# Performance work log

Measured on AMD Instinct MI355X. Metric: run time of the kernel, lower is better.

Reference implementation:

```python
import jax, jax.numpy as jnp
import numpy as np
from jax import lax

ALPHA = 2.0
T_TAGS = 8  # number of distinct connects tags
ANCHOR_POS_FACTOR = jnp.array([1.0, 1.0], dtype=jnp.float32)
POS_FACTOR = [2.0, 1.0]  # [4,4,4,2,1][-2:]
NEG_FACTOR = [2.0, 1.0]


def setup_inputs() -> dict:
    key = jax.random.key(0)
    ks = jax.random.split(key, 10)
    B, A, M = 2, 2, 64
    Da, Db = 128, 64
    logits_a = jax.random.normal(ks[0], (B, A, Da, Da, Da), dtype=jnp.float32)
    logits_b = jax.random.normal(ks[1], (B, A, Db, Db, Db), dtype=jnp.float32)
    # GT prob maps: background labeled -1 (negmask), sparse positives labeled 1
    prob_a = jnp.where(jax.random.uniform(ks[2], (B, A, Da, Da, Da)) < 0.995, -1.0, 1.0).astype(jnp.float32)
    prob_b = jnp.where(jax.random.uniform(ks[3], (B, A, Db, Db, Db)) < 0.995, -1.0, 1.0).astype(jnp.float32)
    connects_a = jax.random.randint(ks[4], (B, A, Da, Da, Da), 0, T_TAGS, dtype=jnp.int32)
    connects_b = jax.random.randint(ks[5], (B, A, Db, Db, Db), 0, T_TAGS, dtype=jnp.int32)
    def make_coord(k, D):
        ka, kz = jax.random.split(k)
        anc = jax.random.randint(ka, (B, M, 1), 0, A, dtype=jnp.int32)
        sp = jax.random.randint(kz, (B, M, 3), 0, D, dtype=jnp.int32)
        c = jnp.concatenate([anc, sp], axis=-1)
        # pad last quarter of rows with -1 (invalid), as in the original padded coord lists
        c = c.at[:, 3 * M // 4:, :].set(-1)
        return c
    coord_a = make_coord(ks[6], Da)
    coord_b = make_coord(ks[7], Db)
    fnames = jnp.arange(B, dtype=jnp.float32)
    return {"logits_a": logits_a, "logits_b": logits_b, "prob_a": prob_a, "prob_b": prob_b,
            "connects_a": connects_a, "connects_b": connects_b,
            "coord_a": coord_a, "coord_b": coord_b, "fnames": fnames}


def _level_loss(logits, prob_gt, connects, coord, pos_f, neg_f):
    # ---- negative branch: sigmoid/logsigmoid elementwise + NMS maxpool mask ----
    prob = jax.nn.sigmoid(logits)
    nll = -jax.nn.log_sigmoid(-logits)  # -log(1 - sigmoid(logit))
    negmask = (prob_gt == -1.0).astype(logits.dtype)
    # max_pool3d kernel 3, stride 1, pad 1 over (D,H,W); anchors are channels
    pooled = lax.reduce_window(prob, -jnp.inf, lax.max,
                               (1, 1, 3, 3, 3), (1, 1, 1, 1, 1), 'SAME')
    max_filter = lax.stop_gradient((pooled == prob).astype(logits.dtype))
    negmask = negmask * max_filter
    w_neg = lax.stop_gradient(prob) ** ALPHA * negmask
    loss_neg = jnp.sum(nll * w_neg) * neg_f
    count_neg = jnp.sum(w_neg)
    wsum_neg = jnp.sum(w_neg) * neg_f

    # ---- positive branch: batched gather at coords (pad rows = -1) ----
    B, M, _ = coord.shape
    valid = coord[:, :, 0] > -1                       # [B, M]
    c = jnp.where(valid[..., None], coord, 0)         # safe indices
    b_idx = jnp.arange(B)[:, None]
    lp = logits[b_idx, c[..., 0], c[..., 1], c[..., 2], c[..., 3]]  # [B, M]
    pp = jax.nn.sigmoid(lp)
    w1 = (1.0 - lax.stop_gradient(pp)) ** ALPHA
    w2 = ANCHOR_POS_FACTOR[c[..., 0]]
    vf = valid.astype(logits.dtype)
    loss_pos = -jnp.sum(jax.nn.log_sigmoid(lp) * w1 * w2 * vf) * pos_f
    count_pos = jnp.sum(w1 * vf)
    wsum_pos = jnp.sum(w1 * w2 * vf) * pos_f

    # ---- connects-tag segment-min grouping (torch.unique + per-tag min) ----
    tags = connects[b_idx, c[..., 0], c[..., 1], c[..., 2], c[..., 3]]  # [B, M]
    seg = (jnp.arange(B, dtype=jnp.int32)[:, None] * T_TAGS + tags).reshape(-1)
    data = jnp.where(valid, w1, jnp.inf).reshape(-1)
    seg_min = jax.ops.segment_min(data, seg, num_segments=B * T_TAGS).reshape(B, T_TAGS)
    seg_min = jnp.where(jnp.isfinite(seg_min), seg_min, -1.0)  # absent tags -> -1 sentinel
    return loss_pos, loss_neg, count_pos, count_neg, wsum_pos, wsum_neg, seg_min


def reference(logits_a, logits_b, prob_a, prob_b, connects_a, connects_b, coord_a, coord_b, fnames):
    ra = _level_loss(logits_a, prob_a, connects_a, coord_a, POS_FACTOR[0], NEG_FACTOR[0])
    rb = _level_loss(logits_b, prob_b, connects_b, coord_b, POS_FACTOR[1], NEG_FACTOR[1])
    cls_loss_pos = ra[0] + rb[0]
    cls_loss_neg = ra[1] + rb[1]
    count_pos = ra[2] + rb[2]
    count_neg = ra[3] + rb[3]
    wsum_pos = ra[4] + rb[4]
    wsum_neg = ra[5] + rb[5]
    # pred_prob summary: per (level, sample, tag) min positive weight; fnames broadcast alongside
    pred_prob_min = jnp.stack([ra[6], rb[6]], axis=0)  # [2, B, T_TAGS]
    return (cls_loss_pos, cls_loss_neg, count_pos, count_neg, wsum_pos, wsum_neg, pred_prob_min)
```

## Files before the change

kernel.cpp:

```cpp
#include <hip/hip_runtime.h>
#include <math.h>


#define NBLK_A 1024
#define NBLK_B 128
#define NBLK_TOTAL (NBLK_A + NBLK_B + 1)

__device__ __forceinline__ float fmax3(float a, float b, float c) {
    return fmaxf(a, fmaxf(b, c));
}

template <int D, int LOG2D, int XQ>
__device__ __forceinline__ void neg_march(
    const float* __restrict__ logits, const float* __restrict__ gt,
    int vol, int z, int y0, int xq, float& loss, float& wsum)
{
    const int x0 = xq << 2;
    const float* vb = logits + (vol << (3 * LOG2D));
    const int zm = z > 0 ? z - 1 : 0;
    const int zp = z < D - 1 ? z + 1 : z;
    const float* pzm = vb + (zm << (2 * LOG2D));
    const float* pz0 = vb + (z << (2 * LOG2D));
    const float* pzp = vb + (zp << (2 * LOG2D));
    const float* pg = gt + (vol << (3 * LOG2D)) + (z << (2 * LOG2D));

    float zw[3][4];
    float cc[2][4];
    float4 gg[2];

#pragma unroll
    for (int s = 0; s < 10; ++s) {
        int yy = y0 - 1 + s;
        yy = yy < 0 ? 0 : (yy > D - 1 ? D - 1 : yy);
        const int ro = (yy << LOG2D) + x0;
        float4 r0 = *(const float4*)(pzm + ro);
        float4 r1 = *(const float4*)(pz0 + ro);
        float4 r2 = *(const float4*)(pzp + ro);
        if (s >= 1 && s <= 8) gg[s & 1] = *(const float4*)(pg + ro);
        zw[s % 3][0] = fmax3(r0.x, r1.x, r2.x);
        zw[s % 3][1] = fmax3(r0.y, r1.y, r2.y);
        zw[s % 3][2] = fmax3(r0.z, r1.z, r2.z);
        zw[s % 3][3] = fmax3(r0.w, r1.w, r2.w);
        cc[s & 1][0] = r1.x; cc[s & 1][1] = r1.y;
        cc[s & 1][2] = r1.z; cc[s & 1][3] = r1.w;
        if (s >= 2) {
            float cz0 = fmax3(zw[0][0], zw[1][0], zw[2][0]);
            float cz1 = fmax3(zw[0][1], zw[1][1], zw[2][1]);
            float cz2 = fmax3(zw[0][2], zw[1][2], zw[2][2]);
            float cz3 = fmax3(zw[0][3], zw[1][3], zw[2][3]);
            float lco = __shfl_up(cz3, 1);   if (xq == 0)      lco = cz0;
            float rco = __shfl_down(cz0, 1); if (xq == XQ - 1) rco = cz3;
            float m0 = fmax3(lco, cz0, cz1);
            float m1 = fmax3(cz0, cz1, cz2);
            float m2 = fmax3(cz1, cz2, cz3);
            float m3 = fmax3(cz2, cz3, rco);
            const float* c = cc[(s - 1) & 1];
            float4 gq = gg[(s - 1) & 1];
            float ms[4] = {m0, m1, m2, m3};
            float gs[4] = {gq.x, gq.y, gq.z, gq.w};
#pragma unroll
            for (int k = 0; k < 4; ++k) {
                if (gs[k] == -1.0f && ms[k] == c[k]) {
                    float e = __expf(c[k]);
                    float u = __builtin_amdgcn_rcpf(1.0f + e);
                    float sc = e * u;
                    float wv = sc * sc;
                    wsum += wv;
                    loss += (-__logf(u)) * wv;
                }
            }
        }
    }
}

__global__ __launch_bounds__(256, 4) void fused_kernel(
    const float* __restrict__ la, const float* __restrict__ lb,
    const float* __restrict__ ga, const float* __restrict__ gb,
    const int* __restrict__ conn_a, const int* __restrict__ conn_b,
    const int* __restrict__ coord_a, const int* __restrict__ coord_b,
    float* __restrict__ ws, float* __restrict__ out)
{
    __shared__ float sred[8];
    __shared__ float w1s[128];
    __shared__ float tgf[128];
    const int bid = blockIdx.x;
    const int t = threadIdx.x;
    float loss = 0.0f, wsum = 0.0f;
    int accIdx = -1;

    if (bid < NBLK_A) {
        accIdx = 0;
        const int vol = bid >> 8;
        const int rem = bid & 255;
        const int zb = rem >> 4, yc = rem & 15;
        neg_march<128, 7, 32>(la, ga, vol, zb * 8 + (t >> 5), yc * 8, t & 31,
                              loss, wsum);
    } else if (bid < NBLK_A + NBLK_B) {
        accIdx = 2;
        const int b2 = bid - NBLK_A;
        const int vol = b2 >> 5;
        const int rem = b2 & 31;
        const int zb = rem >> 3, yc = rem & 7;
        neg_march<64, 6, 16>(lb, gb, vol, zb * 16 + (t >> 4), yc * 8, t & 15,
                             loss, wsum);
    } else {
        for (int level = 0; level < 2; ++level) {
            const float* logits = level ? lb : la;
            const int* conn = level ? conn_b : conn_a;
            const int* coord = level ? coord_b : coord_a;
            const int D = level ? 64 : 128;
            float li = 0.0f, ci = 0.0f;
            if (t < 128) {
                const int* c4 = coord + t * 4;
                int a = c4[0], zz = c4[1], yy = c4[2], xx = c4[3];
                bool valid = a > -1;
                int aa = valid ? a : 0, z2 = valid ? zz : 0,
                    y2 = valid ? yy : 0, x2 = valid ? xx : 0;
                int b = t >> 6;
                int off = (((b * 2 + aa) * D + z2) * D + y2) * D + x2;
                float lp = logits[off];
                int tag = conn[off];
                float s = 1.0f / (1.0f + expf(lp));
                float w1 = s * s;
                float vf = valid ? 1.0f : 0.0f;
                float sp = fmaxf(-lp, 0.0f) + log1pf(expf(-fabsf(lp)));
                li = sp * w1 * vf;
                ci = w1 * vf;
                w1s[t] = w1;
                tgf[t] = (float)(valid ? tag : -1);
            }
            for (int o = 32; o; o >>= 1) {
                li += __shfl_down(li, o);
                ci += __shfl_down(ci, o);
            }
            if ((t & 63) == 0) { sred[t >> 6] = li; sred[4 + (t >> 6)] = ci; }
            __syncthreads();
            if (t == 0) {
                atomicAdd(ws + 4 + 2 * level, sred[0] + sred[1] + sred[2] + sred[3]);
                atomicAdd(ws + 5 + 2 * level, sred[4] + sred[5] + sred[6] + sred[7]);
            }
            if (t < 16) {
                int bb = t >> 3, tg = t & 7;
                float mn = INFINITY;
                for (int i = 0; i < 64; ++i) {
                    int j = bb * 64 + i;
                    if (tgf[j] == (float)tg) mn = fminf(mn, w1s[j]);
                }
                out[6 + level * 16 + bb * 8 + tg] = isinf(mn) ? -1.0f : mn;
            }
            __syncthreads();
        }
    }

    if (accIdx >= 0) {
        for (int o = 32; o; o >>= 1) {
            loss += __shfl_down(loss, o);
            wsum += __shfl_down(wsum, o);
        }
        if ((t & 63) == 0) { sred[t >> 6] = loss; sred[4 + (t >> 6)] = wsum; }
        __syncthreads();
        if (t == 0) {
            float L = sred[0] + sred[1] + sred[2] + sred[3];
            float W = sred[4] + sred[5] + sred[6] + sred[7];
            if (L != 0.0f || W != 0.0f) {
                atomicAdd(ws + accIdx, L);
                atomicAdd(ws + accIdx + 1, W);
            }
        }
    }

    if (t == 0) {
        __threadfence();
        unsigned int old = atomicAdd((unsigned int*)(ws + 8), 1u);
        if (old == NBLK_TOTAL - 1) {
            float s0 = atomicAdd(ws + 0, 0.0f);
            float s1 = atomicAdd(ws + 1, 0.0f);
            float s2 = atomicAdd(ws + 2, 0.0f);
            float s3 = atomicAdd(ws + 3, 0.0f);
            float s4 = atomicAdd(ws + 4, 0.0f);
            float s5 = atomicAdd(ws + 5, 0.0f);
            float s6 = atomicAdd(ws + 6, 0.0f);
            float s7 = atomicAdd(ws + 7, 0.0f);
            out[0] = s4 * 2.0f + s6;
            out[1] = s0 * 2.0f + s2;
            out[2] = s5 + s7;
            out[3] = s1 + s3;
            out[4] = s5 * 2.0f + s7;
            out[5] = s1 * 2.0f + s3;
        }
    }
}

extern "C" void kernel_launch(void* const* d_in, const int* in_sizes, int n_in,
                              void* d_out, int out_size, void* d_ws, size_t ws_size,
                              hipStream_t stream) {
    const float* logits_a = (const float*)d_in[0];
    const float* logits_b = (const float*)d_in[1];
    const float* prob_a   = (const float*)d_in[2];
    const float* prob_b   = (const float*)d_in[3];
    const int*   conn_a   = (const int*)d_in[4];
    const int*   conn_b   = (const int*)d_in[5];
    const int*   coord_a  = (const int*)d_in[6];
    const int*   coord_b  = (const int*)d_in[7];
    float* out = (float*)d_out;
    float* ws  = (float*)d_ws;

    hipMemsetAsync(ws, 0, 12 * sizeof(float), stream);
    fused_kernel<<<NBLK_TOTAL, 256, 0, stream>>>(
        logits_a, logits_b, prob_a, prob_b,
        conn_a, conn_b, coord_a, coord_b, ws, out);
}
```

Measured before the change: 178.5 us.

## Halve rows per thread and issue all row loads up front before max computation

Each thread now handles 4 output rows instead of 8, and the block count doubles to keep full coverage. The sliding-window loop that interleaved loads and compute is replaced by a batch of 18 float4 logit loads plus 4 gt loads issued before any max or loss work. The goal is more memory-level parallelism per thread and more resident blocks to hide latency. In exchange, the halo overhead rises from 10/8 to 6/4 rows loaded per output row, which adds redundant reads, and register pressure increases.

```diff
diff --git a/kernel.cpp b/kernel.cpp
--- a/kernel.cpp
+++ b/kernel.cpp
@@ -2,12 +2,17 @@
 #include <math.h>
 
 
-#define NBLK_A 1024
-#define NBLK_B 128
+#define NBLK_A 2048
+#define NBLK_B 256
 #define NBLK_TOTAL (NBLK_A + NBLK_B + 1)
 
 __device__ __forceinline__ float fmax3(float a, float b, float c) {
     return fmaxf(a, fmaxf(b, c));
+}
+
+__device__ __forceinline__ float4 fmax3v(float4 a, float4 b, float4 c) {
+    return make_float4(fmax3(a.x, b.x, c.x), fmax3(a.y, b.y, c.y),
+                       fmax3(a.z, b.z, c.z), fmax3(a.w, b.w, c.w));
 }
 
 template <int D, int LOG2D, int XQ>
@@ -24,50 +29,48 @@
     const float* pzp = vb + (zp << (2 * LOG2D));
     const float* pg = gt + (vol << (3 * LOG2D)) + (z << (2 * LOG2D));
 
-    float zw[3][4];
-    float cc[2][4];
-    float4 gg[2];
-
-#pragma unroll
-    for (int s = 0; s < 10; ++s) {
+    float4 R[6][3];
+    float4 G[4];
+#pragma unroll
+    for (int s = 0; s < 6; ++s) {
         int yy = y0 - 1 + s;
         yy = yy < 0 ? 0 : (yy > D - 1 ? D - 1 : yy);
         const int ro = (yy << LOG2D) + x0;
-        float4 r0 = *(const float4*)(pzm + ro);
-        float4 r1 = *(const float4*)(pz0 + ro);
-        float4 r2 = *(const float4*)(pzp + ro);
-        if (s >= 1 && s <= 8) gg[s & 1] = *(const float4*)(pg + ro);
-        zw[s % 3][0] = fmax3(r0.x, r1.x, r2.x);
-        zw[s % 3][1] = fmax3(r0.y, r1.y, r2.y);
-        zw[s % 3][2] = fmax3(r0.z, r1.z, r2.z);
-        zw[s % 3][3] = fmax3(r0.w, r1.w, r2.w);
-        cc[s & 1][0] = r1.x; cc[s & 1][1] = r1.y;
-        cc[s & 1][2] = r1.z; cc[s & 1][3] = r1.w;
-        if (s >= 2) {
-            float cz0 = fmax3(zw[0][0], zw[1][0], zw[2][0]);
-            float cz1 = fmax3(zw[0][1], zw[1][1], zw[2][1]);
-            float cz2 = fmax3(zw[0][2], zw[1][2], zw[2][2]);
-            float cz3 = fmax3(zw[0][3], zw[1][3], zw[2][3]);
-            float lco = __shfl_up(cz3, 1);   if (xq == 0)      lco = cz0;
-            float rco = __shfl_down(cz0, 1); if (xq == XQ - 1) rco = cz3;
-            float m0 = fmax3(lco, cz0, cz1);
-            float m1 = fmax3(cz0, cz1, cz2);
-            float m2 = fmax3(cz1, cz2, cz3);
-            float m3 = fmax3(cz2, cz3, rco);
-            const float* c = cc[(s - 1) & 1];
-            float4 gq = gg[(s - 1) & 1];
-            float ms[4] = {m0, m1, m2, m3};
-            float gs[4] = {gq.x, gq.y, gq.z, gq.w};
-#pragma unroll
-            for (int k = 0; k < 4; ++k) {
-                if (gs[k] == -1.0f && ms[k] == c[k]) {
-                    float e = __expf(c[k]);
-                    float u = __builtin_amdgcn_rcpf(1.0f + e);
-                    float sc = e * u;
-                    float wv = sc * sc;
-                    wsum += wv;
-                    loss += (-__logf(u)) * wv;
-                }
+        R[s][0] = *(const float4*)(pzm + ro);
+        R[s][1] = *(const float4*)(pz0 + ro);
+        R[s][2] = *(const float4*)(pzp + ro);
+    }
+#pragma unroll
+    for (int j = 0; j < 4; ++j)
+        G[j] = *(const float4*)(pg + ((y0 + j) << LOG2D) + x0);
+
+    float4 zf[6];
+#pragma unroll
+    for (int s = 0; s < 6; ++s) zf[s] = fmax3v(R[s][0], R[s][1], R[s][2]);
+
+#pragma unroll
+    for (int r = 0; r < 4; ++r) {
+        float4 cz = fmax3v(zf[r], zf[r + 1], zf[r + 2]);
+        float lco = __shfl_up(cz.w, 1);   if (xq == 0)      lco = cz.x;
+        float rco = __shfl_down(cz.x, 1); if (xq == XQ - 1) rco = cz.w;
+        float m0 = fmax3(lco, cz.x, cz.y);
+        float m1 = fmax3(cz.x, cz.y, cz.z);
+        float m2 = fmax3(cz.y, cz.z, cz.w);
+        float m3 = fmax3(cz.z, cz.w, rco);
+        float4 c = R[r + 1][1];
+        float4 gq = G[r];
+        float ms[4] = {m0, m1, m2, m3};
+        float cs[4] = {c.x, c.y, c.z, c.w};
+        float gs[4] = {gq.x, gq.y, gq.z, gq.w};
+#pragma unroll
+        for (int k = 0; k < 4; ++k) {
+            if (gs[k] == -1.0f && ms[k] == cs[k]) {
+                float e = __expf(cs[k]);
+                float u = __builtin_amdgcn_rcpf(1.0f + e);
+                float sc = e * u;
+                float wv = sc * sc;
+                wsum += wv;
+                loss += (-__logf(u)) * wv;
             }
         }
     }
@@ -90,18 +93,18 @@
 
     if (bid < NBLK_A) {
         accIdx = 0;
-        const int vol = bid >> 8;
-        const int rem = bid & 255;
-        const int zb = rem >> 4, yc = rem & 15;
-        neg_march<128, 7, 32>(la, ga, vol, zb * 8 + (t >> 5), yc * 8, t & 31,
+        const int vol = bid >> 9;
+        const int rem = bid & 511;
+        const int zb = rem >> 5, yc = rem & 31;
+        neg_march<128, 7, 32>(la, ga, vol, zb * 8 + (t >> 5), yc * 4, t & 31,
                               loss, wsum);
     } else if (bid < NBLK_A + NBLK_B) {
         accIdx = 2;
         const int b2 = bid - NBLK_A;
-        const int vol = b2 >> 5;
-        const int rem = b2 & 31;
-        const int zb = rem >> 3, yc = rem & 7;
-        neg_march<64, 6, 16>(lb, gb, vol, zb * 16 + (t >> 4), yc * 8, t & 15,
+        const int vol = b2 >> 6;
+        const int rem = b2 & 63;
+        const int zb = rem >> 4, yc = rem & 15;
+        neg_march<64, 6, 16>(lb, gb, vol, zb * 16 + (t >> 4), yc * 4, t & 15,
                              loss, wsum);
     } else {
         for (int level = 0; level < 2; ++level) {
```

Measured after the change: 241.3 us. +35.2%, slower.
